# Optimization experiments

Hardware: AMD Instinct MI355X
Metric: run time of the kernel (lower is better)

The kernel has to match this reference:

```python
import jax, jax.numpy as jnp
import numpy as np

T, N, E = 32, 5000, 80000
F_IN, H, HD, NH, C = 128, 128, 512, 8, 10
DH = H // NH  # head dim
EPS = 1e-5


def _gcn_conv(x, src, dst, W, b):
    n = x.shape[0]
    loops = jnp.arange(n, dtype=src.dtype)
    s = jnp.concatenate([src, loops])
    d = jnp.concatenate([dst, loops])
    deg = jax.ops.segment_sum(jnp.ones_like(d, x.dtype), d, num_segments=n)
    dinv = jnp.where(deg > 0, jax.lax.rsqrt(deg), 0.0)
    h = x @ W  # [n, H]
    norm = dinv[s] * dinv[d]  # [e]
    out = jax.ops.segment_sum(h[s] * norm[:, None], d, num_segments=n)
    return out + b


def _graph_embed(x, ei, W0, b0, W1, b1, W2, b2):
    src, dst = ei[0], ei[1]
    h = jnp.tanh(_gcn_conv(x, src, dst, W0, b0))
    h = jnp.tanh(_gcn_conv(h, src, dst, W1, b1))
    h = jnp.tanh(_gcn_conv(h, src, dst, W2, b2))
    return jnp.sum(h, axis=0)  # SumAggregation over all nodes -> [H]


def _forward(x, edge_index, W0, b0, W1, b1, W2, b2,
             Wq, bq, Wk, bk, Wv, bv, Wo, bo,
             g2, beta2, Wm1, bm1, Wm2, bm2, Wl, bl):
    # per-graph GCN stack + sum aggregation -> [T, H]
    z = jax.vmap(_graph_embed, in_axes=(0, 0) + (None,) * 6)(
        x, edge_index, W0, b0, W1, b1, W2, b2)

    # unbatched multihead self-attention over the T sequence
    q = (z @ Wq + bq).reshape(T, NH, DH)
    k = (z @ Wk + bk).reshape(T, NH, DH)
    v = (z @ Wv + bv).reshape(T, NH, DH)
    scores = jnp.einsum('thd,shd->hts', q, k) / jnp.sqrt(jnp.asarray(DH, z.dtype))
    attn = jax.nn.softmax(scores, axis=-1)
    o = jnp.einsum('hts,shd->thd', attn, v).reshape(T, H)
    x_attend = o @ Wo + bo  # dropout1 is identity in eval
    # NOTE: layer_norm1 output is dead code in the original forward (assigned to x, never used)

    mlp = jax.nn.relu(x_attend @ Wm1 + bm1) @ Wm2 + bm2
    x_attend = x_attend + mlp  # dropout2 identity in eval

    mu = jnp.mean(x_attend, axis=-1, keepdims=True)
    var = jnp.var(x_attend, axis=-1, keepdims=True)
    x_attend = (x_attend - mu) * jax.lax.rsqrt(var + EPS) * g2 + beta2

    pooled = jnp.sum(jax.nn.relu(x_attend), axis=0)  # [H]
    return pooled @ Wl + bl  # [C]


def setup_inputs() -> dict:
    key = jax.random.key(0)
    ks = jax.random.split(key, 24)

    def lin(k, fan_in, shape):
        return jax.random.normal(k, shape, jnp.float32) / np.sqrt(fan_in)

    inp = {
        'x': jax.random.normal(ks[0], (T, N, F_IN), jnp.float32),
        'edge_index': jax.random.randint(ks[1], (T, 2, E), 0, N, jnp.int32),
        'W0': lin(ks[2], F_IN, (F_IN, H)), 'b0': jnp.zeros((H,), jnp.float32),
        'W1': lin(ks[3], H, (H, H)), 'b1': jnp.zeros((H,), jnp.float32),
        'W2': lin(ks[4], H, (H, H)), 'b2': jnp.zeros((H,), jnp.float32),
        'Wq': lin(ks[5], H, (H, H)), 'bq': jnp.zeros((H,), jnp.float32),
        'Wk': lin(ks[6], H, (H, H)), 'bk': jnp.zeros((H,), jnp.float32),
        'Wv': lin(ks[7], H, (H, H)), 'bv': jnp.zeros((H,), jnp.float32),
        'Wo': lin(ks[8], H, (H, H)), 'bo': jnp.zeros((H,), jnp.float32),
        'g2': jnp.ones((H,), jnp.float32), 'beta2': jnp.zeros((H,), jnp.float32),
        'Wm1': lin(ks[9], H, (H, HD)), 'bm1': jnp.zeros((HD,), jnp.float32),
        'Wm2': lin(ks[10], HD, (HD, H)), 'bm2': jnp.zeros((H,), jnp.float32),
        'Wl': lin(ks[11], H, (H, C)), 'bl': jnp.zeros((C,), jnp.float32),
    }
    return inp


def reference(x, edge_index, W0, b0, W1, b1, W2, b2,
              Wq, bq, Wk, bk, Wv, bv, Wo, bo,
              g2, beta2, Wm1, bm1, Wm2, bm2, Wl, bl):
    return _forward(x, edge_index, W0, b0, W1, b1, W2, b2,
                    Wq, bq, Wk, bk, Wv, bv, Wo, bo,
                    g2, beta2, Wm1, bm1, Wm2, bm2, Wl, bl)
```

## Files before the change

### kernel.cpp

```cpp
#include <hip/hip_runtime.h>
#include <cstdint>

#define T_ 32
#define N_ 5000
#define E_ 80000
#define H_ 128
#define HD_ 512
#define C_ 10

typedef _Float16 f16;
typedef f16 f16x8 __attribute__((ext_vector_type(8)));
typedef f16 f16x4 __attribute__((ext_vector_type(4)));
typedef f16 f16x2 __attribute__((ext_vector_type(2)));
typedef float f32x4 __attribute__((ext_vector_type(4)));

#define LDA 136
#define NB_ 8
#define EPS_ (E_ / NB_)
#define STRIPS 16
#define NBLK_ 313

__device__ inline int addpk(int a, int b) {
    f16x2 x = __builtin_bit_cast(f16x2, a);
    f16x2 y = __builtin_bit_cast(f16x2, b);
    f16x2 r = x + y;
    return __builtin_bit_cast(int, r);
}

__device__ inline float fast_tanh(float x) {
    return 1.0f - 2.0f / (__expf(2.0f * x) + 1.0f);
}

__global__ __launch_bounds__(256) void k_count(const int* __restrict__ ei, int* __restrict__ part) {
    __shared__ int cnt[N_];
    int blk = blockIdx.x;
    int t = blk & 31, seg = blk >> 5;
    int tid = threadIdx.x;
    for (int i = tid; i < N_; i += 256) cnt[i] = 0;
    __syncthreads();
    const int* dst = ei + (size_t)t * 2 * E_ + E_ + seg * EPS_;
    for (int e = tid * 4; e < EPS_; e += 1024) {
        int4 d = *(const int4*)&dst[e];
        atomicAdd(&cnt[d.x], 1);
        atomicAdd(&cnt[d.y], 1);
        atomicAdd(&cnt[d.z], 1);
        atomicAdd(&cnt[d.w], 1);
    }
    __syncthreads();
    int* p = part + (t * NB_ + seg) * N_;
    for (int i = tid * 4; i < N_; i += 1024) *(int4*)&p[i] = *(const int4*)&cnt[i];
}

__global__ __launch_bounds__(256) void k_scan(int* __restrict__ part, int* __restrict__ ptr,
                                              float* __restrict__ dinv, float* __restrict__ z) {
    __shared__ int cnt[N_];
    __shared__ int red[256];
    int t = blockIdx.x, tid = threadIdx.x;
    int base = t * N_;
    if (tid < 128) z[t * 128 + tid] = 0.0f;
    int* pp = part + t * NB_ * N_;

    for (int i = tid; i < N_; i += 256) {
        int c = 0;
#pragma unroll
        for (int s = 0; s < NB_; ++s) c += pp[s * N_ + i];
        cnt[i] = c;
        dinv[base + i] = rsqrtf((float)(c + 1));
    }
    __syncthreads();

    int vals[20];
    int sum = 0;
#pragma unroll
    for (int j = 0; j < 20; ++j) {
        int i = tid * 20 + j;
        int c = (i < N_) ? cnt[i] : 0;
        vals[j] = sum;
        sum += c;
    }
    red[tid] = sum;
    __syncthreads();
    for (int off = 1; off < 256; off <<= 1) {
        int v = (tid >= off) ? red[tid - off] : 0;
        __syncthreads();
        red[tid] += v;
        __syncthreads();
    }
    int prev = (tid > 0) ? red[tid - 1] : 0;
#pragma unroll
    for (int j = 0; j < 20; ++j) {
        int i = tid * 20 + j;
        if (i < N_) cnt[i] = prev + vals[j];
    }
    __syncthreads();

    for (int i = tid; i < N_; i += 256) {
        int run = cnt[i];
        ptr[base + i] = run;
#pragma unroll
        for (int s = 0; s < NB_; ++s) {
            int c = pp[s * N_ + i];
            pp[s * N_ + i] = run;
            run += c;
        }
    }
}

__global__ __launch_bounds__(256) void k_scatter(const int* __restrict__ ei,
                                                 const int* __restrict__ part,
                                                 uint16_t* __restrict__ col) {
    __shared__ int cur[N_];
    int blk = blockIdx.x;
    int t = blk & 31, seg = blk >> 5;
    int tid = threadIdx.x;
    const int* off = part + (t * NB_ + seg) * N_;
    for (int i = tid * 4; i < N_; i += 1024) *(int4*)&cur[i] = *(const int4*)&off[i];
    __syncthreads();
    const int* src = ei + (size_t)t * 2 * E_ + seg * EPS_;
    const int* dst = src + E_;
    uint16_t* cl = col + (size_t)t * E_;
    for (int e = tid * 4; e < EPS_; e += 1024) {
        int4 s4 = *(const int4*)&src[e];
        int4 d4 = *(const int4*)&dst[e];
        cl[atomicAdd(&cur[d4.x], 1)] = (uint16_t)s4.x;
        cl[atomicAdd(&cur[d4.y], 1)] = (uint16_t)s4.y;
        cl[atomicAdd(&cur[d4.z], 1)] = (uint16_t)s4.z;
        cl[atomicAdd(&cur[d4.w], 1)] = (uint16_t)s4.w;
    }
}

__global__ __launch_bounds__(256) void k_wprep(const float* __restrict__ W0,
                                               const float* __restrict__ W1,
                                               const float* __restrict__ W2,
                                               f16* __restrict__ Wt) {
    const float* W = (blockIdx.x == 0) ? W0 : (blockIdx.x == 1) ? W1 : W2;
    f16* dst = Wt + blockIdx.x * 16384;
    for (int idx = threadIdx.x; idx < 16384; idx += 256) {
        int c = idx >> 7, k = idx & 127;
        dst[idx] = (f16)W[k * 128 + c];
    }
}

template <bool F32IN>
__global__ __launch_bounds__(256) void k_gemm(const void* __restrict__ in_,
                                              const f16* __restrict__ Wt,
                                              const float* __restrict__ dinv,
                                              f16* __restrict__ g) {
    __shared__ f16 Ws[128 * LDA];
    __shared__ f16 As[64 * LDA];
    int b = blockIdx.x;
    int t = b & 31;
    int strip = b >> 5;
    int tid = threadIdx.x;

    {
        int c = tid >> 1, hf = tid & 1;
        const f16* src = Wt + c * 128 + hf * 64;
        f16* dst = Ws + c * LDA + hf * 64;
#pragma unroll
        for (int j = 0; j < 8; ++j) *(f16x8*)&dst[j * 8] = *(const f16x8*)&src[j * 8];
    }

    int w = tid >> 6, lane = tid & 63;
    int m = lane & 15, q = lane >> 4;
    int rw = w * 16;
    int sr = tid >> 2, skq = (tid & 3) * 32;

    for (int tile = strip; tile < 79; tile += STRIPS) {
        int r0 = tile * 64;
        {
            bool valid = (r0 + sr) < N_;
            f16* dst = As + sr * LDA + skq;
            if (F32IN) {
                const float* src = (const float*)in_ + ((size_t)(t * N_ + r0 + sr)) * H_ + skq;
#pragma unroll
                for (int j = 0; j < 8; ++j) {
                    float4 v = valid ? *(const float4*)&src[j * 4] : make_float4(0.f, 0.f, 0.f, 0.f);
                    dst[j * 4 + 0] = (f16)v.x;
                    dst[j * 4 + 1] = (f16)v.y;
                    dst[j * 4 + 2] = (f16)v.z;
                    dst[j * 4 + 3] = (f16)v.w;
                }
            } else {
                const f16* src = (const f16*)in_ + ((size_t)(t * N_ + r0 + sr)) * H_ + skq;
#pragma unroll
                for (int j = 0; j < 4; ++j) {
                    f16x8 v = {};
                    if (valid) v = *(const f16x8*)&src[j * 8];
                    *(f16x8*)&dst[j * 8] = v;
                }
            }
        }
        __syncthreads();

        f32x4 acc[8];
#pragma unroll
        for (int n = 0; n < 8; ++n) acc[n] = (f32x4){0.f, 0.f, 0.f, 0.f};
#pragma unroll
        for (int kb = 0; kb < 4; ++kb) {
            f16x8 aF = *(const f16x8*)&As[(rw + m) * LDA + kb * 32 + q * 8];
#pragma unroll
            for (int n = 0; n < 8; ++n) {
                f16x8 bF = *(const f16x8*)&Ws[(n * 16 + m) * LDA + kb * 32 + q * 8];
                acc[n] = __builtin_amdgcn_mfma_f32_16x16x32_f16(aF, bF, acc[n], 0, 0, 0);
            }
        }
        __syncthreads();

#pragma unroll
        for (int i = 0; i < 4; ++i) {
            int rr = rw + q * 4 + i;
            int gr = r0 + rr;
            float d = dinv[t * N_ + (gr < N_ ? gr : N_ - 1)];
#pragma unroll
            for (int n = 0; n < 8; ++n)
                As[rr * LDA + n * 16 + m] = (f16)(acc[n][i] * d);
        }
        __syncthreads();
        if (r0 + sr < N_) {
            f16* dst = g + ((size_t)(t * N_ + r0 + sr)) * H_ + skq;
            const f16* src = As + sr * LDA + skq;
#pragma unroll
            for (int j = 0; j < 4; ++j) *(f16x8*)&dst[j * 8] = *(const f16x8*)&src[j * 8];
        }
        __syncthreads();
    }
}

__global__ __launch_bounds__(256) void k_aggr(const int* __restrict__ ptr,
                                              const uint16_t* __restrict__ col,
                                              const f16* __restrict__ g,
                                              const float* __restrict__ dinv,
                                              const float* __restrict__ b,
                                              f16* __restrict__ out) {
    int x = blockIdx.x & 7;
    int j = blockIdx.x >> 3;
    int gsel = j / NBLK_;
    int nb = j - gsel * NBLK_;
    int t = x + (gsel << 3);

    int w = threadIdx.x >> 6;
    int lane = threadIdx.x & 63;
    int q = lane >> 4, m = lane & 15;
    int n0 = nb * 16 + w * 4;
    if (n0 >= N_) return;
    int base = t * N_;
    const f16* gg = g + (size_t)base * H_;
    const uint16_t* cl = col + (size_t)t * E_;
    int n = n0 + q;
    unsigned moB = (unsigned)(m * 8);

    int4 p4 = *(const int4*)&ptr[base + n0];
    int pend = (n0 + 4 < N_) ? ptr[base + n0 + 4] : E_;
    int begin = (q == 0) ? p4.x : (q == 1) ? p4.y : (q == 2) ? p4.z : p4.w;
    int end   = (q == 0) ? p4.y : (q == 1) ? p4.z : (q == 2) ? p4.w : pend;

    float dn = dinv[base + n];
    float4 b4a = *(const float4*)&b[m * 8];
    float4 b4b = *(const float4*)&b[m * 8 + 4];

    int zidx = 320000 - 5000 * t;

    f16x8 a0 = *(const f16x8*)&gg[((unsigned)n << 7) + moB];
    f16x8 a1 = {}, a2 = {}, a3 = {}, a4 = {}, a5 = {}, a6 = {}, a7 = {};

    int e0 = begin & ~7;
    int elast = (end - 1) & ~7;
    unsigned span = (unsigned)(end - begin);
    uint4 cc = *(const uint4*)&cl[e0];
    for (int e = e0; e < end; e += 8) {
        int en = e + 8;
        int epf = en < elast ? en : elast;
        uint4 cn = *(const uint4*)&cl[epf];
        unsigned eb = (unsigned)(e - begin);
        int i0 = (int)(cc.x & 0xFFFFu), i1 = (int)(cc.x >> 16);
        int i2 = (int)(cc.y & 0xFFFFu), i3 = (int)(cc.y >> 16);
        int i4 = (int)(cc.z & 0xFFFFu), i5 = (int)(cc.z >> 16);
        int i6 = (int)(cc.w & 0xFFFFu), i7 = (int)(cc.w >> 16);
        int s0 = (eb + 0 < span) ? i0 : zidx;
        int s1 = (eb + 1 < span) ? i1 : zidx;
        int s2 = (eb + 2 < span) ? i2 : zidx;
        int s3 = (eb + 3 < span) ? i3 : zidx;
        int s4 = (eb + 4 < span) ? i4 : zidx;
        int s5 = (eb + 5 < span) ? i5 : zidx;
        int s6 = (eb + 6 < span) ? i6 : zidx;
        int s7 = (eb + 7 < span) ? i7 : zidx;
        f16x8 v0 = *(const f16x8*)&gg[((unsigned)s0 << 7) + moB];
        f16x8 v1 = *(const f16x8*)&gg[((unsigned)s1 << 7) + moB];
        f16x8 v2 = *(const f16x8*)&gg[((unsigned)s2 << 7) + moB];
        f16x8 v3 = *(const f16x8*)&gg[((unsigned)s3 << 7) + moB];
        f16x8 v4 = *(const f16x8*)&gg[((unsigned)s4 << 7) + moB];
        f16x8 v5 = *(const f16x8*)&gg[((unsigned)s5 << 7) + moB];
        f16x8 v6 = *(const f16x8*)&gg[((unsigned)s6 << 7) + moB];
        f16x8 v7 = *(const f16x8*)&gg[((unsigned)s7 << 7) + moB];
        a0 += v0; a1 += v1; a2 += v2; a3 += v3;
        a4 += v4; a5 += v5; a6 += v6; a7 += v7;
        cc = cn;
    }
    a0 += a1; a2 += a3; a4 += a5; a6 += a7;
    a0 += a2; a4 += a6;
    a0 += a4;

    f16x8 o;
#pragma unroll
    for (int jj = 0; jj < 8; ++jj) {
        float bj = (jj < 4) ? ((const float*)&b4a)[jj] : ((const float*)&b4b)[jj - 4];
        o[jj] = (f16)fast_tanh(dn * (float)a0[jj] + bj);
    }
    *(f16x8*)&out[((size_t)base + n) * H_ + moB] = o;
}

__global__ __launch_bounds__(256) void k_reduce(const f16* __restrict__ h, float* __restrict__ z) {
    int t = blockIdx.x, seg = blockIdx.y;
    int tid = threadIdx.x;
    int rg = tid >> 5;
    int c = (tid & 31) * 4;
    const f16* p = h + (size_t)t * N_ * H_;
    float4 acc = make_float4(0.f, 0.f, 0.f, 0.f);
    int n0 = seg * 500;
    for (int n = n0 + rg; n < n0 + 500; n += 8) {
        f16x4 v = *(const f16x4*)&p[(size_t)n * H_ + c];
        acc.x += (float)v[0]; acc.y += (float)v[1]; acc.z += (float)v[2]; acc.w += (float)v[3];
    }
    __shared__ float4 part[256];
    part[tid] = acc;
    __syncthreads();
    if (rg == 0) {
        float4 s = part[tid];
#pragma unroll
        for (int j = 1; j < 8; ++j) {
            float4 v = part[(j << 5) + tid];
            s.x += v.x; s.y += v.y; s.z += v.z; s.w += v.w;
        }
        atomicAdd(&z[t * H_ + c + 0], s.x);
        atomicAdd(&z[t * H_ + c + 1], s.y);
        atomicAdd(&z[t * H_ + c + 2], s.z);
        atomicAdd(&z[t * H_ + c + 3], s.w);
    }
}

__global__ __launch_bounds__(128) void k_qkv(const float* __restrict__ z,
                                             const float* __restrict__ Wq, const float* __restrict__ bq,
                                             const float* __restrict__ Wk, const float* __restrict__ bk,
                                             const float* __restrict__ Wv, const float* __restrict__ bv,
                                             float* __restrict__ q, float* __restrict__ k,
                                             float* __restrict__ v) {
    int t = blockIdx.x, c = threadIdx.x;
    __shared__ float zs[128];
    zs[c] = z[t * 128 + c];
    __syncthreads();
    float aq = bq[c], ak = bk[c], av = bv[c];
    for (int kk = 0; kk < 128; ++kk) {
        float zv = zs[kk];
        aq += zv * Wq[(kk << 7) + c];
        ak += zv * Wk[(kk << 7) + c];
        av += zv * Wv[(kk << 7) + c];
    }
    q[t * 128 + c] = aq;
    k[t * 128 + c] = ak;
    v[t * 128 + c] = av;
}

__global__ __launch_bounds__(256) void k_attnmid(
    const float* __restrict__ q, const float* __restrict__ k, const float* __restrict__ v,
    const float* __restrict__ Wo, const float* __restrict__ bo,
    const float* __restrict__ g2, const float* __restrict__ beta2,
    const float* __restrict__ Wm1, const float* __restrict__ bm1,
    const float* __restrict__ Wm2, const float* __restrict__ bm2,
    float* __restrict__ xr) {
    int t = blockIdx.x, tid = threadIdx.x;
    __shared__ float Ks[32 * 128], Vs[32 * 128];
    __shared__ float qs[128], sc[8 * 32], xa[128], hid[512], ys[128];
    __shared__ float redA[128], redB[128];

    for (int i = tid; i < 32 * 128; i += 256) { Ks[i] = k[i]; Vs[i] = v[i]; }
    if (tid < 128) qs[tid] = q[t * 128 + tid];
    __syncthreads();

    {
        int h = tid >> 5, s = tid & 31;
        float d = 0.0f;
#pragma unroll
        for (int kk = 0; kk < 16; ++kk)
            d += qs[(h << 4) + kk] * Ks[(s << 7) + (h << 4) + kk];
        sc[tid] = d * 0.25f;
    }
    __syncthreads();
    if (tid < 8) {
        float m = -1e30f;
        for (int s = 0; s < 32; ++s) m = fmaxf(m, sc[(tid << 5) + s]);
        float l = 0.0f;
        for (int s = 0; s < 32; ++s) { float e = __expf(sc[(tid << 5) + s] - m); sc[(tid << 5) + s] = e; l += e; }
        float inv = 1.0f / l;
        for (int s = 0; s < 32; ++s) sc[(tid << 5) + s] *= inv;
    }
    __syncthreads();
    if (tid < 128) {
        int h = tid >> 4;
        float o = 0.0f;
        for (int s = 0; s < 32; ++s) o += sc[(h << 5) + s] * Vs[(s << 7) + tid];
        qs[tid] = o;
    }
    __syncthreads();
    if (tid < 128) {
        float a = bo[tid];
        for (int kk = 0; kk < 128; ++kk) a += qs[kk] * Wo[(kk << 7) + tid];
        xa[tid] = a;
    }
    __syncthreads();
    for (int j = tid; j < 512; j += 256) {
        float a = bm1[j];
        for (int kk = 0; kk < 128; ++kk) a += xa[kk] * Wm1[(kk << 9) + j];
        hid[j] = fmaxf(a, 0.0f);
    }
    __syncthreads();
    if (tid < 128) {
        float a = bm2[tid];
        for (int j = 0; j < 512; ++j) a += hid[j] * Wm2[(j << 7) + tid];
        ys[tid] = xa[tid] + a;
    }
    __syncthreads();
    if (tid < 128) { redA[tid] = ys[tid]; redB[tid] = ys[tid] * ys[tid]; }
    __syncthreads();
    for (int off = 64; off > 0; off >>= 1) {
        if (tid < off) { redA[tid] += redA[tid + off]; redB[tid] += redB[tid + off]; }
        __syncthreads();
    }
    float mu = redA[0] * (1.0f / 128.0f);
    float var = redB[0] * (1.0f / 128.0f) - mu * mu;
    float rs = rsqrtf(var + 1e-5f);
    if (tid < 128) {
        float yv = (ys[tid] - mu) * rs * g2[tid] + beta2[tid];
        xr[t * 128 + tid] = fmaxf(yv, 0.0f);
    }
}

__global__ __launch_bounds__(128) void k_final(const float* __restrict__ xr,
                                               const float* __restrict__ Wl,
                                               const float* __restrict__ bl,
                                               float* __restrict__ out) {
    int tid = threadIdx.x;
    __shared__ float pooled[128];
    float s = 0.0f;
    for (int t = 0; t < 32; ++t) s += xr[t * 128 + tid];
    pooled[tid] = s;
    __syncthreads();
    if (tid < C_) {
        float a = bl[tid];
        for (int kk = 0; kk < 128; ++kk) a += pooled[kk] * Wl[kk * C_ + tid];
        out[tid] = a;
    }
}

extern "C" void kernel_launch(void* const* d_in, const int* in_sizes, int n_in,
                              void* d_out, int out_size, void* d_ws, size_t ws_size,
                              hipStream_t stream) {
    const float* x  = (const float*)d_in[0];
    const int*   ei = (const int*)d_in[1];
    const float* W0 = (const float*)d_in[2];  const float* b0 = (const float*)d_in[3];
    const float* W1 = (const float*)d_in[4];  const float* b1 = (const float*)d_in[5];
    const float* W2 = (const float*)d_in[6];  const float* b2 = (const float*)d_in[7];
    const float* Wq = (const float*)d_in[8];  const float* bq = (const float*)d_in[9];
    const float* Wk = (const float*)d_in[10]; const float* bk = (const float*)d_in[11];
    const float* Wv = (const float*)d_in[12]; const float* bv = (const float*)d_in[13];
    const float* Wo = (const float*)d_in[14]; const float* bo = (const float*)d_in[15];
    const float* g2 = (const float*)d_in[16]; const float* beta2 = (const float*)d_in[17];
    const float* Wm1 = (const float*)d_in[18]; const float* bm1 = (const float*)d_in[19];
    const float* Wm2 = (const float*)d_in[20]; const float* bm2 = (const float*)d_in[21];
    const float* Wl = (const float*)d_in[22]; const float* bl = (const float*)d_in[23];
    float* outp = (float*)d_out;

    const size_t BIG = (size_t)T_ * N_ * H_;
    char* ws = (char*)d_ws;
    float*    dinv = (float*)(ws);
    int*      ptr  = (int*)(ws + 640000);
    uint16_t* col  = (uint16_t*)(ws + 1280000);
    f16*      Wt   = (f16*)(ws + 6400000);
    f16*      P16  = (f16*)(ws + 6498304);
    f16*      Q16  = P16 + BIG;
    float*    z    = (float*)(Q16 + BIG);
    float*    zq   = z + 4096;
    float*    zk   = zq + 4096;
    float*    zv   = zk + 4096;
    float*    xr   = zv + 4096;
    int*      part = (int*)P16;

    k_wprep<<<3, 256, 0, stream>>>(W0, W1, W2, Wt);
    k_count<<<NB_ * 32, 256, 0, stream>>>(ei, part);
    k_scan<<<T_, 256, 0, stream>>>(part, ptr, dinv, z);
    k_scatter<<<NB_ * 32, 256, 0, stream>>>(ei, part, col);

    const float* bl_[3] = {b0, b1, b2};
    const int AGGR_BLOCKS = NBLK_ * 32;
    k_gemm<true><<<STRIPS * 32, 256, 0, stream>>>(x, Wt, dinv, P16);
    k_aggr<<<AGGR_BLOCKS, 256, 0, stream>>>(ptr, col, P16, dinv, bl_[0], Q16);
    k_gemm<false><<<STRIPS * 32, 256, 0, stream>>>(Q16, Wt + 16384, dinv, P16);
    k_aggr<<<AGGR_BLOCKS, 256, 0, stream>>>(ptr, col, P16, dinv, bl_[1], Q16);
    k_gemm<false><<<STRIPS * 32, 256, 0, stream>>>(Q16, Wt + 32768, dinv, P16);
    k_aggr<<<AGGR_BLOCKS, 256, 0, stream>>>(ptr, col, P16, dinv, bl_[2], Q16);

    k_reduce<<<dim3(T_, 10), 256, 0, stream>>>(Q16, z);

    k_qkv<<<T_, 128, 0, stream>>>(z, Wq, bq, Wk, bk, Wv, bv, zq, zk, zv);
    k_attnmid<<<T_, 256, 0, stream>>>(zq, zk, zv, Wo, bo, g2, beta2,
                                      Wm1, bm1, Wm2, bm2, xr);
    k_final<<<1, 128, 0, stream>>>(xr, Wl, bl, outp);
}
```

Before: 521.2 us.

## Prefetch next GEMM tile into registers and raise strip count and occupancy

The GCN feature GEMM now loads the first A tile before its loop. Inside the loop it issues global loads for the next tile into registers before the MFMA compute, then writes them to shared memory after the output store. This hides global load latency behind the compute. STRIPS grows from 16 to 24 to launch more blocks, and launch_bounds asks for 3 blocks per CU, which adds register pressure from the held prefetch values.

```diff
diff --git a/kernel.cpp b/kernel.cpp
--- a/kernel.cpp
+++ b/kernel.cpp
@@ -17,7 +17,7 @@
 #define LDA 136
 #define NB_ 8
 #define EPS_ (E_ / NB_)
-#define STRIPS 16
+#define STRIPS 24
 #define NBLK_ 313
 
 __device__ inline int addpk(int a, int b) {
@@ -142,10 +142,10 @@
 }
 
 template <bool F32IN>
-__global__ __launch_bounds__(256) void k_gemm(const void* __restrict__ in_,
-                                              const f16* __restrict__ Wt,
-                                              const float* __restrict__ dinv,
-                                              f16* __restrict__ g) {
+__global__ __launch_bounds__(256, 3) void k_gemm(const void* __restrict__ in_,
+                                                 const f16* __restrict__ Wt,
+                                                 const float* __restrict__ dinv,
+                                                 f16* __restrict__ g) {
     __shared__ f16 Ws[128 * LDA];
     __shared__ f16 As[64 * LDA];
     int b = blockIdx.x;
@@ -166,32 +166,55 @@
     int rw = w * 16;
     int sr = tid >> 2, skq = (tid & 3) * 32;
 
+    {
+        f16* dst = As + sr * LDA + skq;
+        if (F32IN) {
+            const float* src = (const float*)in_ + ((size_t)(t * N_ + strip * 64 + sr)) * H_ + skq;
+#pragma unroll
+            for (int j = 0; j < 8; ++j) {
+                float4 v = *(const float4*)&src[j * 4];
+                dst[j * 4 + 0] = (f16)v.x;
+                dst[j * 4 + 1] = (f16)v.y;
+                dst[j * 4 + 2] = (f16)v.z;
+                dst[j * 4 + 3] = (f16)v.w;
+            }
+        } else {
+            const f16* src = (const f16*)in_ + ((size_t)(t * N_ + strip * 64 + sr)) * H_ + skq;
+#pragma unroll
+            for (int j = 0; j < 4; ++j) *(f16x8*)&dst[j * 8] = *(const f16x8*)&src[j * 8];
+        }
+    }
+    __syncthreads();
+
     for (int tile = strip; tile < 79; tile += STRIPS) {
         int r0 = tile * 64;
-        {
-            bool valid = (r0 + sr) < N_;
-            f16* dst = As + sr * LDA + skq;
+        int tn = tile + STRIPS;
+        bool havn = tn < 79;
+
+        float4 nf0, nf1, nf2, nf3, nf4, nf5, nf6, nf7;
+        f16x8 nh0, nh1, nh2, nh3;
+        if (havn) {
+            bool valid = (tn * 64 + sr) < N_;
             if (F32IN) {
-                const float* src = (const float*)in_ + ((size_t)(t * N_ + r0 + sr)) * H_ + skq;
-#pragma unroll
-                for (int j = 0; j < 8; ++j) {
-                    float4 v = valid ? *(const float4*)&src[j * 4] : make_float4(0.f, 0.f, 0.f, 0.f);
-                    dst[j * 4 + 0] = (f16)v.x;
-                    dst[j * 4 + 1] = (f16)v.y;
-                    dst[j * 4 + 2] = (f16)v.z;
-                    dst[j * 4 + 3] = (f16)v.w;
-                }
+                const float* src = (const float*)in_ + ((size_t)(t * N_ + tn * 64 + sr)) * H_ + skq;
+                float4 zz = make_float4(0.f, 0.f, 0.f, 0.f);
+                nf0 = valid ? *(const float4*)&src[0]  : zz;
+                nf1 = valid ? *(const float4*)&src[4]  : zz;
+                nf2 = valid ? *(const float4*)&src[8]  : zz;
+                nf3 = valid ? *(const float4*)&src[12] : zz;
+                nf4 = valid ? *(const float4*)&src[16] : zz;
+                nf5 = valid ? *(const float4*)&src[20] : zz;
+                nf6 = valid ? *(const float4*)&src[24] : zz;
+                nf7 = valid ? *(const float4*)&src[28] : zz;
             } else {
-                const f16* src = (const f16*)in_ + ((size_t)(t * N_ + r0 + sr)) * H_ + skq;
-#pragma unroll
-                for (int j = 0; j < 4; ++j) {
-                    f16x8 v = {};
-                    if (valid) v = *(const f16x8*)&src[j * 8];
-                    *(f16x8*)&dst[j * 8] = v;
-                }
+                const f16* src = (const f16*)in_ + ((size_t)(t * N_ + tn * 64 + sr)) * H_ + skq;
+                f16x8 zz = {};
+                nh0 = valid ? *(const f16x8*)&src[0]  : zz;
+                nh1 = valid ? *(const f16x8*)&src[8]  : zz;
+                nh2 = valid ? *(const f16x8*)&src[16] : zz;
+                nh3 = valid ? *(const f16x8*)&src[24] : zz;
             }
         }
-        __syncthreads();
 
         f32x4 acc[8];
 #pragma unroll
@@ -222,6 +245,25 @@
             const f16* src = As + sr * LDA + skq;
 #pragma unroll
             for (int j = 0; j < 4; ++j) *(f16x8*)&dst[j * 8] = *(const f16x8*)&src[j * 8];
+        }
+        __syncthreads();
+        if (havn) {
+            f16* dst = As + sr * LDA + skq;
+            if (F32IN) {
+                dst[0]  = (f16)nf0.x; dst[1]  = (f16)nf0.y; dst[2]  = (f16)nf0.z; dst[3]  = (f16)nf0.w;
+                dst[4]  = (f16)nf1.x; dst[5]  = (f16)nf1.y; dst[6]  = (f16)nf1.z; dst[7]  = (f16)nf1.w;
+                dst[8]  = (f16)nf2.x; dst[9]  = (f16)nf2.y; dst[10] = (f16)nf2.z; dst[11] = (f16)nf2.w;
+                dst[12] = (f16)nf3.x; dst[13] = (f16)nf3.y; dst[14] = (f16)nf3.z; dst[15] = (f16)nf3.w;
+                dst[16] = (f16)nf4.x; dst[17] = (f16)nf4.y; dst[18] = (f16)nf4.z; dst[19] = (f16)nf4.w;
+                dst[20] = (f16)nf5.x; dst[21] = (f16)nf5.y; dst[22] = (f16)nf5.z; dst[23] = (f16)nf5.w;
+                dst[24] = (f16)nf6.x; dst[25] = (f16)nf6.y; dst[26] = (f16)nf6.z; dst[27] = (f16)nf6.w;
+                dst[28] = (f16)nf7.x; dst[29] = (f16)nf7.y; dst[30] = (f16)nf7.z; dst[31] = (f16)nf7.w;
+            } else {
+                *(f16x8*)&dst[0]  = nh0;
+                *(f16x8*)&dst[8]  = nh1;
+                *(f16x8*)&dst[16] = nh2;
+                *(f16x8*)&dst[24] = nh3;
+            }
         }
         __syncthreads();
     }
```

Measured after the change: 531.1 us. About the same (+1.9%).

## Restructure GCN GEMM into per-wave 16-row tasks loading A directly to registers

Applied to the files above, without the earlier changes.

The dense feature-transform GEMM no longer stages a 64-row A tile through shared memory with block-wide barriers; each wave instead handles an independent 16-row task, loading its A fragments straight from global memory into registers (converting fp32 to fp16 inline for the first layer). Output goes through a private per-wave LDS slab synchronised only with a waitcnt, removing the __syncthreads between load, compute and store. The grid changes to 768 blocks with a launch-bounds occupancy hint, and tasks are ordered by graph group to match the aggregation kernel's ordering. The cost is less A reuse through LDS and more per-wave global loads with a strided access pattern.

```diff
diff --git a/kernel.cpp b/kernel.cpp
--- a/kernel.cpp
+++ b/kernel.cpp
@@ -17,8 +17,8 @@
 #define LDA 136
 #define NB_ 8
 #define EPS_ (E_ / NB_)
-#define STRIPS 16
 #define NBLK_ 313
+#define GEMMB 768
 
 __device__ inline int addpk(int a, int b) {
     f16x2 x = __builtin_bit_cast(f16x2, a);
@@ -29,6 +29,11 @@
 
 __device__ inline float fast_tanh(float x) {
     return 1.0f - 2.0f / (__expf(2.0f * x) + 1.0f);
+}
+
+__device__ inline f16x8 cvt8(float4 a, float4 b) {
+    return (f16x8){(f16)a.x, (f16)a.y, (f16)a.z, (f16)a.w,
+                   (f16)b.x, (f16)b.y, (f16)b.z, (f16)b.w};
 }
 
 __global__ __launch_bounds__(256) void k_count(const int* __restrict__ ei, int* __restrict__ part) {
@@ -142,17 +147,13 @@
 }
 
 template <bool F32IN>
-__global__ __launch_bounds__(256) void k_gemm(const void* __restrict__ in_,
-                                              const f16* __restrict__ Wt,
-                                              const float* __restrict__ dinv,
-                                              f16* __restrict__ g) {
+__global__ __launch_bounds__(256, 3) void k_gemm(const void* __restrict__ in_,
+                                                 const f16* __restrict__ Wt,
+                                                 const float* __restrict__ dinv,
+                                                 f16* __restrict__ g) {
     __shared__ f16 Ws[128 * LDA];
-    __shared__ f16 As[64 * LDA];
-    int b = blockIdx.x;
-    int t = b & 31;
-    int strip = b >> 5;
+    __shared__ f16 slab[4][16 * LDA];
     int tid = threadIdx.x;
-
     {
         int c = tid >> 1, hf = tid & 1;
         const f16* src = Wt + c * 128 + hf * 64;
@@ -160,70 +161,86 @@
 #pragma unroll
         for (int j = 0; j < 8; ++j) *(f16x8*)&dst[j * 8] = *(const f16x8*)&src[j * 8];
     }
-
+    __syncthreads();
+
+    int xc = blockIdx.x & 7;
+    int jb = blockIdx.x >> 3;
     int w = tid >> 6, lane = tid & 63;
     int m = lane & 15, q = lane >> 4;
-    int rw = w * 16;
-    int sr = tid >> 2, skq = (tid & 3) * 32;
-
-    for (int tile = strip; tile < 79; tile += STRIPS) {
-        int r0 = tile * 64;
-        {
-            bool valid = (r0 + sr) < N_;
-            f16* dst = As + sr * LDA + skq;
-            if (F32IN) {
-                const float* src = (const float*)in_ + ((size_t)(t * N_ + r0 + sr)) * H_ + skq;
-#pragma unroll
-                for (int j = 0; j < 8; ++j) {
-                    float4 v = valid ? *(const float4*)&src[j * 4] : make_float4(0.f, 0.f, 0.f, 0.f);
-                    dst[j * 4 + 0] = (f16)v.x;
-                    dst[j * 4 + 1] = (f16)v.y;
-                    dst[j * 4 + 2] = (f16)v.z;
-                    dst[j * 4 + 3] = (f16)v.w;
-                }
-            } else {
-                const f16* src = (const f16*)in_ + ((size_t)(t * N_ + r0 + sr)) * H_ + skq;
-#pragma unroll
-                for (int j = 0; j < 4; ++j) {
-                    f16x8 v = {};
-                    if (valid) v = *(const f16x8*)&src[j * 8];
-                    *(f16x8*)&dst[j * 8] = v;
-                }
-            }
-        }
-        __syncthreads();
+    int co = q * 8;
+    f16* sl = slab[w];
+    int srow = lane >> 4;
+    int scol = (lane & 15) * 8;
+
+    for (int task = jb * 4 + w; task < 4 * NBLK_; task += 384) {
+        int gsel = task / NBLK_;
+        int tile = task - gsel * NBLK_;
+        int t = xc + (gsel << 3);
+        int base = t * N_;
+        int r0 = tile * 16;
+        int rowA = r0 + m; if (rowA >= N_) rowA = N_ - 1;
+
+        f16x8 a0, a1, a2, a3;
+        if (F32IN) {
+            const float* src = (const float*)in_ + (((size_t)(base + rowA)) << 7) + co;
+            float4 u0 = *(const float4*)&src[0];
+            float4 u1 = *(const float4*)&src[4];
+            float4 u2 = *(const float4*)&src[32];
+            float4 u3 = *(const float4*)&src[36];
+            float4 u4 = *(const float4*)&src[64];
+            float4 u5 = *(const float4*)&src[68];
+            float4 u6 = *(const float4*)&src[96];
+            float4 u7 = *(const float4*)&src[100];
+            a0 = cvt8(u0, u1); a1 = cvt8(u2, u3); a2 = cvt8(u4, u5); a3 = cvt8(u6, u7);
+        } else {
+            const f16* src = (const f16*)in_ + (((size_t)(base + rowA)) << 7) + co;
+            a0 = *(const f16x8*)&src[0];
+            a1 = *(const f16x8*)&src[32];
+            a2 = *(const f16x8*)&src[64];
+            a3 = *(const f16x8*)&src[96];
+        }
 
         f32x4 acc[8];
 #pragma unroll
         for (int n = 0; n < 8; ++n) acc[n] = (f32x4){0.f, 0.f, 0.f, 0.f};
 #pragma unroll
-        for (int kb = 0; kb < 4; ++kb) {
-            f16x8 aF = *(const f16x8*)&As[(rw + m) * LDA + kb * 32 + q * 8];
-#pragma unroll
-            for (int n = 0; n < 8; ++n) {
-                f16x8 bF = *(const f16x8*)&Ws[(n * 16 + m) * LDA + kb * 32 + q * 8];
-                acc[n] = __builtin_amdgcn_mfma_f32_16x16x32_f16(aF, bF, acc[n], 0, 0, 0);
-            }
-        }
-        __syncthreads();
+        for (int n = 0; n < 8; ++n) {
+            f16x8 bF = *(const f16x8*)&Ws[(n * 16 + m) * LDA + co];
+            acc[n] = __builtin_amdgcn_mfma_f32_16x16x32_f16(a0, bF, acc[n], 0, 0, 0);
+        }
+#pragma unroll
+        for (int n = 0; n < 8; ++n) {
+            f16x8 bF = *(const f16x8*)&Ws[(n * 16 + m) * LDA + 32 + co];
+            acc[n] = __builtin_amdgcn_mfma_f32_16x16x32_f16(a1, bF, acc[n], 0, 0, 0);
+        }
+#pragma unroll
+        for (int n = 0; n < 8; ++n) {
+            f16x8 bF = *(const f16x8*)&Ws[(n * 16 + m) * LDA + 64 + co];
+            acc[n] = __builtin_amdgcn_mfma_f32_16x16x32_f16(a2, bF, acc[n], 0, 0, 0);
+        }
+#pragma unroll
+        for (int n = 0; n < 8; ++n) {
+            f16x8 bF = *(const f16x8*)&Ws[(n * 16 + m) * LDA + 96 + co];
+            acc[n] = __builtin_amdgcn_mfma_f32_16x16x32_f16(a3, bF, acc[n], 0, 0, 0);
+        }
 
 #pragma unroll
         for (int i = 0; i < 4; ++i) {
-            int rr = rw + q * 4 + i;
-            int gr = r0 + rr;
-            float d = dinv[t * N_ + (gr < N_ ? gr : N_ - 1)];
+            int rr = q * 4 + i;
+            int gr = r0 + rr; if (gr >= N_) gr = N_ - 1;
+            float d = dinv[base + gr];
 #pragma unroll
             for (int n = 0; n < 8; ++n)
-                As[rr * LDA + n * 16 + m] = (f16)(acc[n][i] * d);
-        }
-        __syncthreads();
-        if (r0 + sr < N_) {
-            f16* dst = g + ((size_t)(t * N_ + r0 + sr)) * H_ + skq;
-            const f16* src = As + sr * LDA + skq;
-#pragma unroll
-            for (int j = 0; j < 4; ++j) *(f16x8*)&dst[j * 8] = *(const f16x8*)&src[j * 8];
-        }
-        __syncthreads();
+                sl[rr * LDA + n * 16 + m] = (f16)(acc[n][i] * d);
+        }
+        asm volatile("s_waitcnt lgkmcnt(0)" ::: "memory");
+#pragma unroll
+        for (int j4 = 0; j4 < 4; ++j4) {
+            int row = j4 * 4 + srow;
+            f16x8 v = *(const f16x8*)&sl[row * LDA + scol];
+            if (r0 + row < N_)
+                *(f16x8*)&g[(((size_t)(base + r0 + row)) << 7) + scol] = v;
+        }
     }
 }
 
@@ -492,11 +509,11 @@
 
     const float* bl_[3] = {b0, b1, b2};
     const int AGGR_BLOCKS = NBLK_ * 32;
-    k_gemm<true><<<STRIPS * 32, 256, 0, stream>>>(x, Wt, dinv, P16);
+    k_gemm<true><<<GEMMB, 256, 0, stream>>>(x, Wt, dinv, P16);
     k_aggr<<<AGGR_BLOCKS, 256, 0, stream>>>(ptr, col, P16, dinv, bl_[0], Q16);
-    k_gemm<false><<<STRIPS * 32, 256, 0, stream>>>(Q16, Wt + 16384, dinv, P16);
+    k_gemm<false><<<GEMMB, 256, 0, stream>>>(Q16, Wt + 16384, dinv, P16);
     k_aggr<<<AGGR_BLOCKS, 256, 0, stream>>>(ptr, col, P16, dinv, bl_[1], Q16);
-    k_gemm<false><<<STRIPS * 32, 256, 0, stream>>>(Q16, Wt + 32768, dinv, P16);
+    k_gemm<false><<<GEMMB, 256, 0, stream>>>(Q16, Wt + 32768, dinv, P16);
     k_aggr<<<AGGR_BLOCKS, 256, 0, stream>>>(ptr, col, P16, dinv, bl_[2], Q16);
 
     k_reduce<<<dim3(T_, 10), 256, 0, stream>>>(Q16, z);
```

New measurement: 488.5 us. -6.3%, faster.
